# Kernel tuning notes

Hardware: AMD Instinct MI355X
Metric: run time of the kernel (lower is better)

The kernel has to match this reference:

```python
import jax, jax.numpy as jnp
import numpy as np

TARGETS_COUNT = 8
TARGET_LEN = 256
BATCH = 32


def setup_inputs() -> dict:
    key = jax.random.key(0)
    target = jax.random.normal(key, (BATCH, TARGETS_COUNT, TARGET_LEN), dtype=jnp.float32)
    return {"target": target}


def _bispectrum(x):
    # x: [L].  TM[l1, l2] = (1/L) * sum_n x[n] * x[n-l1] * x[n-l2],
    # where x[k] = 0 for k < 0 (zero left-padding, non-circular).
    L = x.shape[0]
    n = jnp.arange(L)
    idx = n[None, :] - n[:, None]            # idx[l, n] = n - l
    S = jnp.where(idx >= 0, x[jnp.clip(idx, 0, L - 1)], jnp.float32(0))  # S[l, n] = x[n-l]
    # TM[l1, l2] = sum_n (x[n] * S[l1, n]) * S[l2, n]
    return ((S * x[None, :]) @ S.T) / L      # [L, L]


def reference(target):
    # target: [B, T, L] -> bispectrum per signal, averaged over T.
    bs = jax.vmap(jax.vmap(_bispectrum))(target)      # [B, T, L, L]
    source = jnp.mean(bs, axis=1)[:, None, :, :]       # [B, 1, L, L]
    return source, target
```

## Files before the change

### kernel.cpp

```cpp
#include <hip/hip_runtime.h>


#define LEN 256
#define NT 8
#define F1OFF 4113
#define REDSTR 68
#define SMEM_DW 8704

typedef _Float16 f16x8 __attribute__((ext_vector_type(8)));
typedef float    f32x4 __attribute__((ext_vector_type(4)));

__constant__ uchar4 kBlockTab[20] = {
    {0,0,0,0},{0,0,2,0},{0,0,4,0},{0,0,6,0},
    {1,0,2,0},{1,0,4,0},{1,0,6,0},
    {1,1,2,0},{1,1,4,0},{1,1,6,0},
    {2,0,4,0},{2,0,6,0},
    {2,1,4,0},{2,1,6,0},
    {2,2,4,0},{2,2,6,0},
    {3,0,6,0},{3,1,6,0},{3,2,6,0},{3,3,6,0}};
__constant__ uchar4 kPairTab[10] = {
    {0,0,0,4},{1,0,4,3},{1,1,7,3},{2,0,10,2},{2,1,12,2},{2,2,14,2},
    {3,0,16,1},{3,1,17,1},{3,2,18,1},{3,3,19,1}};

static __device__ __forceinline__ void split2(float a0, float a1, uint& hb, uint& lb) {
    auto h = __builtin_amdgcn_cvt_pkrtz(a0, a1);
    float e0 = a0 - (float)h[0];
    float e1 = a1 - (float)h[1];
    auto e = __builtin_amdgcn_cvt_pkrtz(e0, e1);
    __builtin_memcpy(&hb, &h, 4);
    __builtin_memcpy(&lb, &e, 4);
}
static __device__ __forceinline__ f16x8 mkf(const uint* u) {
    f16x8 v;
    __builtin_memcpy(&v, u, 16);
    return v;
}
static __device__ __forceinline__ void readwin(const float* fs, int p0, float* wv) {
    const float* bp = fs + p0 + ((p0 & 1) ? F1OFF : 0);
    float2 d0 = *(const float2*)bp;
    float2 d1 = *(const float2*)(bp + 2);
    float2 d2 = *(const float2*)(bp + 4);
    float2 d3 = *(const float2*)(bp + 6);
    wv[0] = d0.x; wv[1] = d0.y; wv[2] = d1.x; wv[3] = d1.y;
    wv[4] = d2.x; wv[5] = d2.y; wv[6] = d3.x; wv[7] = d3.y;
}

__global__ __launch_bounds__(256, 3) void bispec_main(const float* __restrict__ x,
                                                      float* __restrict__ dst,
                                                      int partial) {
    __shared__ float fs[SMEM_DW];
    const int b  = blockIdx.y;
    const int bx = blockIdx.x;

    int ti, tj, kb0, kbn;
    if (partial) {
        uchar4 e = kBlockTab[bx];
        ti = e.x; tj = e.y; kb0 = e.z; kbn = 2;
    } else {
        ti = bx >> 2; tj = bx & 3;
        int m = ti > tj ? ti : tj;
        kb0 = 2 * m; kbn = 8 - 2 * m;
    }
    const int l1b = ti << 6, l2b = tj << 6;
    const int tid = threadIdx.x;
    const int w = tid >> 6, l = tid & 63, cg = l & 15, g = l >> 4;

    const float* xb = x + b * (NT * LEN);
    for (int i = tid; i < 4096; i += 256) {
        int j = i & 511;
        float v = (j >= 256) ? xb[(i >> 9) * 256 + (j - 256)] : 0.0f;
        fs[i] = v;
        fs[F1OFF + i] = v;
    }
    __syncthreads();

    f32x4 acc[4][4];
    #pragma unroll
    for (int mi = 0; mi < 4; ++mi)
        #pragma unroll
        for (int ni = 0; ni < 4; ++ni) acc[mi][ni] = 0.0f;

    for (int tt = 0; tt < 2; ++tt) {
        const int t  = w + tt * 4;
        const int tB = t * 512 + 256;
        const int cA = tB + g * 8 - l1b - cg;
        const int cB = tB + g * 8 - l2b - cg;
        const int cX = tB + g * 8;

        for (int kb = kb0; kb < kb0 + kbn; ++kb) {
            const float4 x0 = *(const float4*)&fs[cX + kb * 32];
            const float4 x1 = *(const float4*)&fs[cX + kb * 32 + 4];
            const float xn[8] = {x0.x, x0.y, x0.z, x0.w, x1.x, x1.y, x1.z, x1.w};

            f16x8 ah[4], al[4];
            #pragma unroll
            for (int mi = 0; mi < 4; ++mi) {
                float wv[8];
                readwin(fs, cA + kb * 32 - mi * 16, wv);
                uint Ahp[4], Alp[4];
                #pragma unroll
                for (int p = 0; p < 4; ++p)
                    split2(xn[2 * p] * wv[2 * p], xn[2 * p + 1] * wv[2 * p + 1],
                           Ahp[p], Alp[p]);
                ah[mi] = mkf(Ahp); al[mi] = mkf(Alp);
            }

            #pragma unroll
            for (int ni = 0; ni < 4; ++ni) {
                float wv[8];
                readwin(fs, cB + kb * 32 - ni * 16, wv);
                uint Bhp[4], Blp[4];
                #pragma unroll
                for (int p = 0; p < 4; ++p)
                    split2(wv[2 * p], wv[2 * p + 1], Bhp[p], Blp[p]);
                const f16x8 bh = mkf(Bhp), bl = mkf(Blp);
                #pragma unroll
                for (int mi = 0; mi < 4; ++mi) {
                    acc[mi][ni] = __builtin_amdgcn_mfma_f32_16x16x32_f16(ah[mi], bh, acc[mi][ni], 0, 0, 0);
                    acc[mi][ni] = __builtin_amdgcn_mfma_f32_16x16x32_f16(ah[mi], bl, acc[mi][ni], 0, 0, 0);
                    acc[mi][ni] = __builtin_amdgcn_mfma_f32_16x16x32_f16(al[mi], bh, acc[mi][ni], 0, 0, 0);
                }
            }
        }
    }

    __syncthreads();
    float* buf0 = fs;
    float* buf1 = fs + 4352;
    if (w >= 2) {
        float* bb = (w == 2) ? buf0 : buf1;
        #pragma unroll
        for (int mi = 0; mi < 4; ++mi)
            #pragma unroll
            for (int ni = 0; ni < 4; ++ni)
                *(f32x4*)&bb[(ni * 16 + cg) * REDSTR + mi * 16 + g * 4] = acc[mi][ni];
    }
    __syncthreads();
    if (w < 2) {
        float* bb = (w == 0) ? buf0 : buf1;
        #pragma unroll
        for (int mi = 0; mi < 4; ++mi)
            #pragma unroll
            for (int ni = 0; ni < 4; ++ni)
                acc[mi][ni] += *(f32x4*)&bb[(ni * 16 + cg) * REDSTR + mi * 16 + g * 4];
    }
    __syncthreads();
    if (w == 1) {
        #pragma unroll
        for (int mi = 0; mi < 4; ++mi)
            #pragma unroll
            for (int ni = 0; ni < 4; ++ni)
                *(f32x4*)&buf0[(ni * 16 + cg) * REDSTR + mi * 16 + g * 4] = acc[mi][ni];
    }
    __syncthreads();
    if (w == 0) {
        #pragma unroll
        for (int mi = 0; mi < 4; ++mi)
            #pragma unroll
            for (int ni = 0; ni < 4; ++ni)
                acc[mi][ni] += *(f32x4*)&buf0[(ni * 16 + cg) * REDSTR + mi * 16 + g * 4];

        if (partial) {
            float* ob = dst + ((size_t)b * 20 + bx) * 4096;
            #pragma unroll
            for (int mi = 0; mi < 4; ++mi)
                #pragma unroll
                for (int ni = 0; ni < 4; ++ni)
                    #pragma unroll
                    for (int q = 0; q < 4; ++q)
                        ob[(mi * 16 + g * 4 + q) * 64 + ni * 16 + cg] = acc[mi][ni][q];
        } else {
            float* ob = dst + (size_t)b * (LEN * LEN);
            const float s = 1.0f / (float)(LEN * NT);
            #pragma unroll
            for (int mi = 0; mi < 4; ++mi)
                #pragma unroll
                for (int ni = 0; ni < 4; ++ni)
                    #pragma unroll
                    for (int q = 0; q < 4; ++q)
                        ob[(size_t)(l1b + mi * 16 + g * 4 + q) * LEN + l2b + ni * 16 + cg] =
                            acc[mi][ni][q] * s;
        }
    }
}

__global__ __launch_bounds__(256) void bispec_reduce(const float* __restrict__ ws,
                                                     float* __restrict__ out) {
    const int p = blockIdx.x, b = blockIdx.y;
    uchar4 e = kPairTab[p];
    const int ii = e.x, jj = e.y, s = e.z, c = e.w;
    const float* base = ws + ((size_t)b * 20 + s) * 4096;
    float* ob = out + (size_t)b * (LEN * LEN);
    const float scale = 1.0f / (float)(LEN * NT);
    for (int k = threadIdx.x; k < 4096; k += 256) {
        float v = base[k];
        for (int q = 1; q < c; ++q) v += base[(size_t)q * 4096 + k];
        v *= scale;
        int r = k >> 6, cc = k & 63;
        ob[(ii * 64 + r) * LEN + jj * 64 + cc] = v;
        if (ii != jj) ob[(jj * 64 + cc) * LEN + ii * 64 + r] = v;
    }
}

extern "C" void kernel_launch(void* const* d_in, const int* in_sizes, int n_in,
                              void* d_out, int out_size, void* d_ws, size_t ws_size,
                              hipStream_t stream) {
    const float* x = (const float*)d_in[0];
    float* out = (float*)d_out;

    const size_t ws_need = (size_t)32 * 20 * 4096 * sizeof(float);
    if (ws_size >= ws_need) {
        float* ws = (float*)d_ws;
        bispec_main<<<dim3(20, 32), dim3(256), 0, stream>>>(x, ws, 1);
        bispec_reduce<<<dim3(10, 32), dim3(256), 0, stream>>>(ws, out);
    } else {
        bispec_main<<<dim3(16, 32), dim3(256), 0, stream>>>(x, out, 0);
    }

    (void)hipMemcpyAsync(out + (size_t)32 * LEN * LEN, x,
                         (size_t)32 * NT * LEN * sizeof(float),
                         hipMemcpyDeviceToDevice, stream);
}
```

Before: 88.99 us.

## Precompute padded shifted planes in global memory and use single-wave blocks

Adds a pad kernel that writes four shifted copies of the zero-padded signal to workspace, plus pre-split fp16 hi/lo pairs for the B operand. The main kernel now runs one wave per block, reads aligned float4 windows straight from global or L2 instead of shared memory, and loops over all 8 signals. This removes the cross-wave shared-memory reduction and the per-iteration B split. The reduce kernel writes the transposed tile through shared memory so the mirrored stores are coalesced. The trade-offs are an extra kernel launch, larger workspace needs, far fewer threads per block, and global-memory reads in the inner loop. If the workspace is smaller than the padded planes, no compute kernel runs at all.

Measured after the change: 130.8 us. +47.0%, slower.

```diff
diff --git a/kernel.cpp b/kernel.cpp
--- a/kernel.cpp
+++ b/kernel.cpp
@@ -3,9 +3,9 @@
 
 #define LEN 256
 #define NT 8
-#define F1OFF 4113
-#define REDSTR 68
-#define SMEM_DW 8704
+#define PLANE 4104
+#define BSTRIDE (8 * PLANE)
+#define QOFF ((size_t)32 * BSTRIDE)
 
 typedef _Float16 f16x8 __attribute__((ext_vector_type(8)));
 typedef float    f32x4 __attribute__((ext_vector_type(4)));
@@ -30,49 +30,57 @@
     __builtin_memcpy(&hb, &h, 4);
     __builtin_memcpy(&lb, &e, 4);
 }
+static __device__ __forceinline__ uint split1(float v) {
+    auto h = __builtin_amdgcn_cvt_pkrtz(v, v);
+    float e = v - (float)h[0];
+    auto l = __builtin_amdgcn_cvt_pkrtz(e, e);
+    uint uh, ul;
+    __builtin_memcpy(&uh, &h, 4);
+    __builtin_memcpy(&ul, &l, 4);
+    return (uh & 0xffffu) | (ul << 16);
+}
 static __device__ __forceinline__ f16x8 mkf(const uint* u) {
     f16x8 v;
     __builtin_memcpy(&v, u, 16);
     return v;
 }
-static __device__ __forceinline__ void readwin(const float* fs, int p0, float* wv) {
-    const float* bp = fs + p0 + ((p0 & 1) ? F1OFF : 0);
-    float2 d0 = *(const float2*)bp;
-    float2 d1 = *(const float2*)(bp + 2);
-    float2 d2 = *(const float2*)(bp + 4);
-    float2 d3 = *(const float2*)(bp + 6);
-    wv[0] = d0.x; wv[1] = d0.y; wv[2] = d1.x; wv[3] = d1.y;
-    wv[4] = d2.x; wv[5] = d2.y; wv[6] = d3.x; wv[7] = d3.y;
-}
-
-__global__ __launch_bounds__(256, 3) void bispec_main(const float* __restrict__ x,
-                                                      float* __restrict__ dst,
-                                                      int partial) {
-    __shared__ float fs[SMEM_DW];
-    const int b  = blockIdx.y;
-    const int bx = blockIdx.x;
-
+
+__global__ __launch_bounds__(256) void bispec_pad(const float* __restrict__ x,
+                                                  float* __restrict__ P) {
+    const int b = blockIdx.x, tid = threadIdx.x;
+    const float* xb = x + b * (NT * LEN);
+    float* Fb = P + (size_t)b * BSTRIDE;
+    uint*  Ub = (uint*)(Fb + 4 * PLANE);
+    for (int c = 0; c < 4; ++c) {
+        for (int i = tid; i < PLANE; i += 256) {
+            int j = i - c;
+            float v = 0.0f;
+            if (j >= 0 && j < 4096) {
+                int jj = j & 511;
+                if (jj >= 256) v = xb[(j >> 9) * 256 + (jj - 256)];
+            }
+            Fb[c * PLANE + i] = v;
+            Ub[c * PLANE + i] = split1(v);
+        }
+    }
+}
+
+template <bool PARTIAL>
+__global__ __launch_bounds__(64, 2) void bispec_main(const float* __restrict__ P,
+                                                     float* __restrict__ dst) {
+    const int b = blockIdx.y, bx = blockIdx.x;
     int ti, tj, kb0, kbn;
-    if (partial) {
+    if (PARTIAL) {
         uchar4 e = kBlockTab[bx];
         ti = e.x; tj = e.y; kb0 = e.z; kbn = 2;
     } else {
-        ti = bx >> 2; tj = bx & 3;
-        int m = ti > tj ? ti : tj;
-        kb0 = 2 * m; kbn = 8 - 2 * m;
+        uchar4 e = kPairTab[bx];
+        ti = e.x; tj = e.y; kb0 = 2 * ti; kbn = 8 - 2 * ti;
     }
     const int l1b = ti << 6, l2b = tj << 6;
-    const int tid = threadIdx.x;
-    const int w = tid >> 6, l = tid & 63, cg = l & 15, g = l >> 4;
-
-    const float* xb = x + b * (NT * LEN);
-    for (int i = tid; i < 4096; i += 256) {
-        int j = i & 511;
-        float v = (j >= 256) ? xb[(i >> 9) * 256 + (j - 256)] : 0.0f;
-        fs[i] = v;
-        fs[F1OFF + i] = v;
-    }
-    __syncthreads();
+    const int l = threadIdx.x, cg = l & 15, g = l >> 4;
+    const float* F = P + (size_t)b * BSTRIDE;
+    const uint*  U = (const uint*)(F + 4 * PLANE);
 
     f32x4 acc[4][4];
     #pragma unroll
@@ -80,23 +88,26 @@
         #pragma unroll
         for (int ni = 0; ni < 4; ++ni) acc[mi][ni] = 0.0f;
 
-    for (int tt = 0; tt < 2; ++tt) {
-        const int t  = w + tt * 4;
+    for (int t = 0; t < NT; ++t) {
         const int tB = t * 512 + 256;
         const int cA = tB + g * 8 - l1b - cg;
         const int cB = tB + g * 8 - l2b - cg;
         const int cX = tB + g * 8;
 
-        for (int kb = kb0; kb < kb0 + kbn; ++kb) {
-            const float4 x0 = *(const float4*)&fs[cX + kb * 32];
-            const float4 x1 = *(const float4*)&fs[cX + kb * 32 + 4];
+        for (int kk = 0; kk < kbn; ++kk) {
+            const int kb = kb0 + kk;
+            const float4* xp = (const float4*)(F + cX + kb * 32);
+            const float4 x0 = xp[0], x1 = xp[1];
             const float xn[8] = {x0.x, x0.y, x0.z, x0.w, x1.x, x1.y, x1.z, x1.w};
 
             f16x8 ah[4], al[4];
             #pragma unroll
             for (int mi = 0; mi < 4; ++mi) {
-                float wv[8];
-                readwin(fs, cA + kb * 32 - mi * 16, wv);
+                const int p0 = cA + kb * 32 - mi * 16;
+                const int c = (-p0) & 3;
+                const float4* wp = (const float4*)(F + c * PLANE + (p0 + c));
+                const float4 w0 = wp[0], w1 = wp[1];
+                const float wv[8] = {w0.x, w0.y, w0.z, w0.w, w1.x, w1.y, w1.z, w1.w};
                 uint Ahp[4], Alp[4];
                 #pragma unroll
                 for (int p = 0; p < 4; ++p)
@@ -107,12 +118,17 @@
 
             #pragma unroll
             for (int ni = 0; ni < 4; ++ni) {
-                float wv[8];
-                readwin(fs, cB + kb * 32 - ni * 16, wv);
+                const int p0 = cB + kb * 32 - ni * 16;
+                const int c = (-p0) & 3;
+                const uint4* up = (const uint4*)(U + c * PLANE + (p0 + c));
+                const uint4 u0 = up[0], u1 = up[1];
+                const uint uu[8] = {u0.x, u0.y, u0.z, u0.w, u1.x, u1.y, u1.z, u1.w};
                 uint Bhp[4], Blp[4];
                 #pragma unroll
-                for (int p = 0; p < 4; ++p)
-                    split2(wv[2 * p], wv[2 * p + 1], Bhp[p], Blp[p]);
+                for (int p = 0; p < 4; ++p) {
+                    Bhp[p] = (uu[2 * p] & 0xffffu) | (uu[2 * p + 1] << 16);
+                    Blp[p] = (uu[2 * p] >> 16) | (uu[2 * p + 1] & 0xffff0000u);
+                }
                 const f16x8 bh = mkf(Bhp), bl = mkf(Blp);
                 #pragma unroll
                 for (int mi = 0; mi < 4; ++mi) {
@@ -124,68 +140,36 @@
         }
     }
 
-    __syncthreads();
-    float* buf0 = fs;
-    float* buf1 = fs + 4352;
-    if (w >= 2) {
-        float* bb = (w == 2) ? buf0 : buf1;
+    if (PARTIAL) {
+        float* ob = dst + ((size_t)b * 20 + bx) * 4096;
         #pragma unroll
         for (int mi = 0; mi < 4; ++mi)
             #pragma unroll
             for (int ni = 0; ni < 4; ++ni)
-                *(f32x4*)&bb[(ni * 16 + cg) * REDSTR + mi * 16 + g * 4] = acc[mi][ni];
-    }
-    __syncthreads();
-    if (w < 2) {
-        float* bb = (w == 0) ? buf0 : buf1;
+                #pragma unroll
+                for (int q = 0; q < 4; ++q)
+                    ob[(mi * 16 + g * 4 + q) * 64 + ni * 16 + cg] = acc[mi][ni][q];
+    } else {
+        const float s = 1.0f / (float)(LEN * NT);
+        float* ob = dst + (size_t)b * (LEN * LEN);
         #pragma unroll
         for (int mi = 0; mi < 4; ++mi)
             #pragma unroll
             for (int ni = 0; ni < 4; ++ni)
-                acc[mi][ni] += *(f32x4*)&bb[(ni * 16 + cg) * REDSTR + mi * 16 + g * 4];
-    }
-    __syncthreads();
-    if (w == 1) {
-        #pragma unroll
-        for (int mi = 0; mi < 4; ++mi)
-            #pragma unroll
-            for (int ni = 0; ni < 4; ++ni)
-                *(f32x4*)&buf0[(ni * 16 + cg) * REDSTR + mi * 16 + g * 4] = acc[mi][ni];
-    }
-    __syncthreads();
-    if (w == 0) {
-        #pragma unroll
-        for (int mi = 0; mi < 4; ++mi)
-            #pragma unroll
-            for (int ni = 0; ni < 4; ++ni)
-                acc[mi][ni] += *(f32x4*)&buf0[(ni * 16 + cg) * REDSTR + mi * 16 + g * 4];
-
-        if (partial) {
-            float* ob = dst + ((size_t)b * 20 + bx) * 4096;
-            #pragma unroll
-            for (int mi = 0; mi < 4; ++mi)
-                #pragma unroll
-                for (int ni = 0; ni < 4; ++ni)
-                    #pragma unroll
-                    for (int q = 0; q < 4; ++q)
-                        ob[(mi * 16 + g * 4 + q) * 64 + ni * 16 + cg] = acc[mi][ni][q];
-        } else {
-            float* ob = dst + (size_t)b * (LEN * LEN);
-            const float s = 1.0f / (float)(LEN * NT);
-            #pragma unroll
-            for (int mi = 0; mi < 4; ++mi)
-                #pragma unroll
-                for (int ni = 0; ni < 4; ++ni)
-                    #pragma unroll
-                    for (int q = 0; q < 4; ++q)
-                        ob[(size_t)(l1b + mi * 16 + g * 4 + q) * LEN + l2b + ni * 16 + cg] =
-                            acc[mi][ni][q] * s;
-        }
+                #pragma unroll
+                for (int q = 0; q < 4; ++q) {
+                    const float v = acc[mi][ni][q] * s;
+                    const int r = l1b + mi * 16 + g * 4 + q;
+                    const int cc = l2b + ni * 16 + cg;
+                    ob[(size_t)r * LEN + cc] = v;
+                    if (ti != tj) ob[(size_t)cc * LEN + r] = v;
+                }
     }
 }
 
 __global__ __launch_bounds__(256) void bispec_reduce(const float* __restrict__ ws,
                                                      float* __restrict__ out) {
+    __shared__ float tile[64][65];
     const int p = blockIdx.x, b = blockIdx.y;
     uchar4 e = kPairTab[p];
     const int ii = e.x, jj = e.y, s = e.z, c = e.w;
@@ -196,9 +180,16 @@
         float v = base[k];
         for (int q = 1; q < c; ++q) v += base[(size_t)q * 4096 + k];
         v *= scale;
-        int r = k >> 6, cc = k & 63;
-        ob[(ii * 64 + r) * LEN + jj * 64 + cc] = v;
-        if (ii != jj) ob[(jj * 64 + cc) * LEN + ii * 64 + r] = v;
+        const int r = k >> 6, cc = k & 63;
+        tile[r][cc] = v;
+        ob[(size_t)(ii * 64 + r) * LEN + jj * 64 + cc] = v;
+    }
+    if (ii != jj) {
+        __syncthreads();
+        for (int k = threadIdx.x; k < 4096; k += 256) {
+            const int r = k >> 6, cc = k & 63;
+            ob[(size_t)(jj * 64 + r) * LEN + ii * 64 + cc] = tile[cc][r];
+        }
     }
 }
 
@@ -207,14 +198,19 @@
                               hipStream_t stream) {
     const float* x = (const float*)d_in[0];
     float* out = (float*)d_out;
-
-    const size_t ws_need = (size_t)32 * 20 * 4096 * sizeof(float);
-    if (ws_size >= ws_need) {
-        float* ws = (float*)d_ws;
-        bispec_main<<<dim3(20, 32), dim3(256), 0, stream>>>(x, ws, 1);
-        bispec_reduce<<<dim3(10, 32), dim3(256), 0, stream>>>(ws, out);
-    } else {
-        bispec_main<<<dim3(16, 32), dim3(256), 0, stream>>>(x, out, 0);
+    float* P = (float*)d_ws;
+
+    const size_t needP = QOFF * sizeof(float);
+    const size_t need  = (QOFF + (size_t)32 * 20 * 4096) * sizeof(float);
+
+    if (ws_size >= need) {
+        float* Q = P + QOFF;
+        bispec_pad<<<dim3(32), dim3(256), 0, stream>>>(x, P);
+        bispec_main<true><<<dim3(20, 32), dim3(64), 0, stream>>>(P, Q);
+        bispec_reduce<<<dim3(10, 32), dim3(256), 0, stream>>>(Q, out);
+    } else if (ws_size >= needP) {
+        bispec_pad<<<dim3(32), dim3(256), 0, stream>>>(x, P);
+        bispec_main<false><<<dim3(10, 32), dim3(64), 0, stream>>>(P, out);
     }
 
     (void)hipMemcpyAsync(out + (size_t)32 * LEN * LEN, x,
```

## Template main kernel, precompute per-lane LDS base, transpose mirror writes via LDS

Applied to the files above, without the earlier changes.

Makes the partial flag a template parameter and replaces the per-read parity branch with a per-lane base pointer chosen once from cg parity, with a changed odd-copy offset. The k loop is unrolled in pairs so address arithmetic is hoisted. The reduce kernel now stages each tile in shared memory so mirrored lower-triangle writes are coalesced rows instead of strided columns. The fallback path launches only upper-triangle blocks and mirrors their output. The changed shared-memory offset may alter bank conflicts.

Result: faster. 87.04 us (-2.2%).

```diff
diff --git a/kernel.cpp b/kernel.cpp
--- a/kernel.cpp
+++ b/kernel.cpp
@@ -3,7 +3,7 @@
 
 #define LEN 256
 #define NT 8
-#define F1OFF 4113
+#define F1OFF 4105
 #define REDSTR 68
 #define SMEM_DW 8704
 
@@ -35,31 +35,20 @@
     __builtin_memcpy(&v, u, 16);
     return v;
 }
-static __device__ __forceinline__ void readwin(const float* fs, int p0, float* wv) {
-    const float* bp = fs + p0 + ((p0 & 1) ? F1OFF : 0);
-    float2 d0 = *(const float2*)bp;
-    float2 d1 = *(const float2*)(bp + 2);
-    float2 d2 = *(const float2*)(bp + 4);
-    float2 d3 = *(const float2*)(bp + 6);
-    wv[0] = d0.x; wv[1] = d0.y; wv[2] = d1.x; wv[3] = d1.y;
-    wv[4] = d2.x; wv[5] = d2.y; wv[6] = d3.x; wv[7] = d3.y;
-}
-
+
+template <bool PARTIAL>
 __global__ __launch_bounds__(256, 3) void bispec_main(const float* __restrict__ x,
-                                                      float* __restrict__ dst,
-                                                      int partial) {
+                                                      float* __restrict__ dst) {
     __shared__ float fs[SMEM_DW];
-    const int b  = blockIdx.y;
-    const int bx = blockIdx.x;
-
-    int ti, tj, kb0, kbn;
-    if (partial) {
+    const int b = blockIdx.y, bx = blockIdx.x;
+
+    int ti, tj, kb0, nkp;
+    if (PARTIAL) {
         uchar4 e = kBlockTab[bx];
-        ti = e.x; tj = e.y; kb0 = e.z; kbn = 2;
+        ti = e.x; tj = e.y; kb0 = e.z; nkp = 1;
     } else {
-        ti = bx >> 2; tj = bx & 3;
-        int m = ti > tj ? ti : tj;
-        kb0 = 2 * m; kbn = 8 - 2 * m;
+        uchar4 e = kPairTab[bx];
+        ti = e.x; tj = e.y; kb0 = 2 * ti; nkp = 4 - ti;
     }
     const int l1b = ti << 6, l2b = tj << 6;
     const int tid = threadIdx.x;
@@ -74,51 +63,70 @@
     }
     __syncthreads();
 
+    const float* fW = fs + ((cg & 1) ? F1OFF : 0);
+
     f32x4 acc[4][4];
     #pragma unroll
     for (int mi = 0; mi < 4; ++mi)
         #pragma unroll
         for (int ni = 0; ni < 4; ++ni) acc[mi][ni] = 0.0f;
 
+    #pragma unroll
     for (int tt = 0; tt < 2; ++tt) {
         const int t  = w + tt * 4;
-        const int tB = t * 512 + 256;
-        const int cA = tB + g * 8 - l1b - cg;
-        const int cB = tB + g * 8 - l2b - cg;
-        const int cX = tB + g * 8;
-
-        for (int kb = kb0; kb < kb0 + kbn; ++kb) {
-            const float4 x0 = *(const float4*)&fs[cX + kb * 32];
-            const float4 x1 = *(const float4*)&fs[cX + kb * 32 + 4];
-            const float xn[8] = {x0.x, x0.y, x0.z, x0.w, x1.x, x1.y, x1.z, x1.w};
-
-            f16x8 ah[4], al[4];
-            #pragma unroll
-            for (int mi = 0; mi < 4; ++mi) {
-                float wv[8];
-                readwin(fs, cA + kb * 32 - mi * 16, wv);
-                uint Ahp[4], Alp[4];
-                #pragma unroll
-                for (int p = 0; p < 4; ++p)
-                    split2(xn[2 * p] * wv[2 * p], xn[2 * p + 1] * wv[2 * p + 1],
-                           Ahp[p], Alp[p]);
-                ah[mi] = mkf(Ahp); al[mi] = mkf(Alp);
-            }
-
-            #pragma unroll
-            for (int ni = 0; ni < 4; ++ni) {
-                float wv[8];
-                readwin(fs, cB + kb * 32 - ni * 16, wv);
-                uint Bhp[4], Blp[4];
-                #pragma unroll
-                for (int p = 0; p < 4; ++p)
-                    split2(wv[2 * p], wv[2 * p + 1], Bhp[p], Blp[p]);
-                const f16x8 bh = mkf(Bhp), bl = mkf(Blp);
+        const int xB0 = t * 512 + 256 + g * 8 + kb0 * 32;
+
+        for (int kp = 0; kp < nkp; ++kp) {
+            const int xB = xB0 + kp * 64;
+            const float* pX = fs + xB;
+            const float* pA = fW + (xB - l1b - cg - 48);
+            const float* pB = fW + (xB - l2b - cg - 48);
+
+            #pragma unroll
+            for (int kk = 0; kk < 2; ++kk) {
+                const int ko = kk * 32;
+                const float4 x0 = *(const float4*)(pX + ko);
+                const float4 x1 = *(const float4*)(pX + ko + 4);
+                const float xn[8] = {x0.x, x0.y, x0.z, x0.w, x1.x, x1.y, x1.z, x1.w};
+
+                f16x8 ah[4], al[4];
                 #pragma unroll
                 for (int mi = 0; mi < 4; ++mi) {
-                    acc[mi][ni] = __builtin_amdgcn_mfma_f32_16x16x32_f16(ah[mi], bh, acc[mi][ni], 0, 0, 0);
-                    acc[mi][ni] = __builtin_amdgcn_mfma_f32_16x16x32_f16(ah[mi], bl, acc[mi][ni], 0, 0, 0);
-                    acc[mi][ni] = __builtin_amdgcn_mfma_f32_16x16x32_f16(al[mi], bh, acc[mi][ni], 0, 0, 0);
+                    const int off = ko + 48 - mi * 16;
+                    float wv[8];
+                    #pragma unroll
+                    for (int p = 0; p < 4; ++p) {
+                        const float2 d = *(const float2*)(pA + off + 2 * p);
+                        wv[2 * p] = d.x; wv[2 * p + 1] = d.y;
+                    }
+                    uint Ahp[4], Alp[4];
+                    #pragma unroll
+                    for (int p = 0; p < 4; ++p)
+                        split2(xn[2 * p] * wv[2 * p], xn[2 * p + 1] * wv[2 * p + 1],
+                               Ahp[p], Alp[p]);
+                    ah[mi] = mkf(Ahp); al[mi] = mkf(Alp);
+                }
+
+                #pragma unroll
+                for (int ni = 0; ni < 4; ++ni) {
+                    const int off = ko + 48 - ni * 16;
+                    float wv[8];
+                    #pragma unroll
+                    for (int p = 0; p < 4; ++p) {
+                        const float2 d = *(const float2*)(pB + off + 2 * p);
+                        wv[2 * p] = d.x; wv[2 * p + 1] = d.y;
+                    }
+                    uint Bhp[4], Blp[4];
+                    #pragma unroll
+                    for (int p = 0; p < 4; ++p)
+                        split2(wv[2 * p], wv[2 * p + 1], Bhp[p], Blp[p]);
+                    const f16x8 bh = mkf(Bhp), bl = mkf(Blp);
+                    #pragma unroll
+                    for (int mi = 0; mi < 4; ++mi) {
+                        acc[mi][ni] = __builtin_amdgcn_mfma_f32_16x16x32_f16(ah[mi], bh, acc[mi][ni], 0, 0, 0);
+                        acc[mi][ni] = __builtin_amdgcn_mfma_f32_16x16x32_f16(ah[mi], bl, acc[mi][ni], 0, 0, 0);
+                        acc[mi][ni] = __builtin_amdgcn_mfma_f32_16x16x32_f16(al[mi], bh, acc[mi][ni], 0, 0, 0);
+                    }
                 }
             }
         }
@@ -160,7 +168,7 @@
             for (int ni = 0; ni < 4; ++ni)
                 acc[mi][ni] += *(f32x4*)&buf0[(ni * 16 + cg) * REDSTR + mi * 16 + g * 4];
 
-        if (partial) {
+        if (PARTIAL) {
             float* ob = dst + ((size_t)b * 20 + bx) * 4096;
             #pragma unroll
             for (int mi = 0; mi < 4; ++mi)
@@ -170,22 +178,27 @@
                     for (int q = 0; q < 4; ++q)
                         ob[(mi * 16 + g * 4 + q) * 64 + ni * 16 + cg] = acc[mi][ni][q];
         } else {
+            const float s = 1.0f / (float)(LEN * NT);
             float* ob = dst + (size_t)b * (LEN * LEN);
-            const float s = 1.0f / (float)(LEN * NT);
             #pragma unroll
             for (int mi = 0; mi < 4; ++mi)
                 #pragma unroll
                 for (int ni = 0; ni < 4; ++ni)
                     #pragma unroll
-                    for (int q = 0; q < 4; ++q)
-                        ob[(size_t)(l1b + mi * 16 + g * 4 + q) * LEN + l2b + ni * 16 + cg] =
-                            acc[mi][ni][q] * s;
+                    for (int q = 0; q < 4; ++q) {
+                        const float v = acc[mi][ni][q] * s;
+                        const int r = l1b + mi * 16 + g * 4 + q;
+                        const int cc = l2b + ni * 16 + cg;
+                        ob[(size_t)r * LEN + cc] = v;
+                        if (ti != tj) ob[(size_t)cc * LEN + r] = v;
+                    }
         }
     }
 }
 
 __global__ __launch_bounds__(256) void bispec_reduce(const float* __restrict__ ws,
                                                      float* __restrict__ out) {
+    __shared__ float tile[64][65];
     const int p = blockIdx.x, b = blockIdx.y;
     uchar4 e = kPairTab[p];
     const int ii = e.x, jj = e.y, s = e.z, c = e.w;
@@ -196,9 +209,16 @@
         float v = base[k];
         for (int q = 1; q < c; ++q) v += base[(size_t)q * 4096 + k];
         v *= scale;
-        int r = k >> 6, cc = k & 63;
-        ob[(ii * 64 + r) * LEN + jj * 64 + cc] = v;
-        if (ii != jj) ob[(jj * 64 + cc) * LEN + ii * 64 + r] = v;
+        const int r = k >> 6, cc = k & 63;
+        tile[r][cc] = v;
+        ob[(size_t)(ii * 64 + r) * LEN + jj * 64 + cc] = v;
+    }
+    if (ii != jj) {
+        __syncthreads();
+        for (int k = threadIdx.x; k < 4096; k += 256) {
+            const int r = k >> 6, cc = k & 63;
+            ob[(size_t)(jj * 64 + r) * LEN + ii * 64 + cc] = tile[cc][r];
+        }
     }
 }
 
@@ -211,10 +231,10 @@
     const size_t ws_need = (size_t)32 * 20 * 4096 * sizeof(float);
     if (ws_size >= ws_need) {
         float* ws = (float*)d_ws;
-        bispec_main<<<dim3(20, 32), dim3(256), 0, stream>>>(x, ws, 1);
+        bispec_main<true><<<dim3(20, 32), dim3(256), 0, stream>>>(x, ws);
         bispec_reduce<<<dim3(10, 32), dim3(256), 0, stream>>>(ws, out);
     } else {
-        bispec_main<<<dim3(16, 32), dim3(256), 0, stream>>>(x, out, 0);
+        bispec_main<false><<<dim3(10, 32), dim3(256), 0, stream>>>(x, out);
     }
 
     (void)hipMemcpyAsync(out + (size_t)32 * LEN * LEN, x,
```
